# Optimization experiments

Hardware: AMD Instinct MI355X
Metric: run time of the kernel (lower is better)

## Reference

```python
import jax, jax.numpy as jnp
import numpy as np

N_NODES = 50000


def gcn_norm(edge_index, edge_weight, n):
    """PyG GCNConv normalization: add self-loops (weight 1), sym-normalize."""
    src, dst = edge_index[0], edge_index[1]
    loop = jnp.arange(n, dtype=src.dtype)
    src = jnp.concatenate([src, loop])
    dst = jnp.concatenate([dst, loop])
    w = jnp.concatenate([edge_weight, jnp.ones((n,), dtype=edge_weight.dtype)])
    deg = jax.ops.segment_sum(w, dst, num_segments=n)  # in-degree w/ self-loops
    dis = jnp.where(deg > 0, jax.lax.rsqrt(deg), 0.0)  # deg^{-1/2}, inf -> 0
    norm = dis[src] * w * dis[dst]                      # [E+N]
    return src, dst, norm


def gcn_conv(x, src, dst, norm, W, b):
    h = x @ W                                            # [N, F_out]
    msg = norm[:, None] * h[src]                         # gather + scale
    out = jax.ops.segment_sum(msg, dst, num_segments=x.shape[0])  # scatter-add
    return out + b


def setup_inputs() -> dict:
    key = jax.random.key(0)
    ks = jax.random.split(key, 10)
    n, e = N_NODES, 800000
    in_dim, hidden, out_dim = 256, 128, 64
    x = jax.random.normal(ks[0], (n, in_dim), dtype=jnp.float32)
    edge_index = jax.random.randint(ks[1], (2, e), 0, n, dtype=jnp.int32)
    edge_weight = jax.random.uniform(ks[2], (e,), dtype=jnp.float32)
    def glorot(k, fi, fo):
        lim = float(np.sqrt(6.0 / (fi + fo)))
        return jax.random.uniform(k, (fi, fo), minval=-lim, maxval=lim, dtype=jnp.float32)
    return {
        "x": x, "edge_index": edge_index, "edge_weight": edge_weight,
        "W1": glorot(ks[3], in_dim, hidden), "b1": jnp.zeros((hidden,), jnp.float32),
        "W2": glorot(ks[4], hidden, hidden), "b2": jnp.zeros((hidden,), jnp.float32),
        "W3": glorot(ks[5], hidden, out_dim), "b3": jnp.zeros((out_dim,), jnp.float32),
    }


def reference(x, edge_index, edge_weight, W1, b1, W2, b2, W3, b3):
    n = x.shape[0]
    src, dst, norm = gcn_norm(edge_index, edge_weight, n)  # cached=True: shared
    h = jax.nn.relu(gcn_conv(x, src, dst, norm, W1, b1))   # dropout: eval mode no-op
    h = jax.nn.relu(gcn_conv(h, src, dst, norm, W2, b2))
    h = gcn_conv(h, src, dst, norm, W3, b3)
    return h
```

## Files before the change

### kernel.cpp

```cpp
#include <hip/hip_runtime.h>
#include <hip/hip_bf16.h>
#include <stdint.h>

#define NODES 50000
#define EDGES 800000
#define R_REP 8
#define DEG_EPT 4
#define SCAN_TB 256
#define SCAN_NB ((NODES + SCAN_TB - 1) / SCAN_TB)

typedef short bf16x8 __attribute__((ext_vector_type(8)));
typedef float f32x4 __attribute__((ext_vector_type(4)));

__device__ __forceinline__ unsigned short f2bf(float f) {
    union { float f; unsigned u; } v; v.f = f;
    unsigned r = v.u + 0x7fff + ((v.u >> 16) & 1);
    return (unsigned short)(r >> 16);
}
__device__ __forceinline__ float bf2f(unsigned short h) {
    union { float f; unsigned u; } v; v.u = ((unsigned)h) << 16;
    return v.f;
}
__device__ __forceinline__ float bflo(unsigned hv) {
    union { float f; unsigned u; } v; v.u = hv << 16;
    return v.f;
}
__device__ __forceinline__ float bfhi(unsigned hv) {
    union { float f; unsigned u; } v; v.u = hv & 0xffff0000u;
    return v.f;
}


__device__ __forceinline__ void wfrag_one(const float* __restrict__ W, unsigned short* Wf,
                                          int idx, int K, int Nn) {
    int NT = Nn >> 4;
    int lane = idx & 63;
    int f = idx >> 6;
    int nt = f % NT;
    int k0 = (f / NT) << 5;
    int n = (nt << 4) + (lane & 15);
    int kk = k0 + ((lane >> 4) << 3);
    unsigned short o[8];
#pragma unroll
    for (int j = 0; j < 8; j++) o[j] = f2bf(W[(kk + j) * Nn + n]);
    ((uint4*)Wf)[idx] = *(uint4*)o;
}

__global__ void k_setup(unsigned long long* packed,
                        const float* __restrict__ W1, unsigned short* Wf1,
                        const float* __restrict__ W2, unsigned short* Wf2,
                        const float* __restrict__ W3, unsigned short* Wf3) {
    int idx = blockIdx.x * blockDim.x + threadIdx.x;
    if (idx < NODES * R_REP) { packed[idx] = 0ull; return; }
    int k = idx - NODES * R_REP;
    if (k < 4096) wfrag_one(W1, Wf1, k, 256, 128);
    else if (k < 6144) wfrag_one(W2, Wf2, k - 4096, 128, 128);
    else if (k < 7168) wfrag_one(W3, Wf3, k - 6144, 128, 64);
}

__global__ void k_deg(const int* __restrict__ dst, const float* __restrict__ w,
                      unsigned long long* __restrict__ packed, int* __restrict__ rank) {
    int base = blockIdx.x * (256 * DEG_EPT) + threadIdx.x;
    int r = blockIdx.x & (R_REP - 1);
    unsigned long long olds[DEG_EPT];
#pragma unroll
    for (int q = 0; q < DEG_EPT; q++) {
        int e = base + q * 256;
        if (e < EDGES) {
            int d = dst[e];
            unsigned fx = __float2uint_rn(w[e] * 16777216.0f);
            unsigned long long add = (1ull << 40) | (unsigned long long)fx;
            olds[q] = atomicAdd(&packed[(size_t)r * NODES + d], add);
        }
    }
#pragma unroll
    for (int q = 0; q < DEG_EPT; q++) {
        int e = base + q * 256;
        if (e < EDGES) rank[e] = (int)(olds[q] >> 40);
    }
}


__global__ void k_scan1(const unsigned long long* __restrict__ packed,
                        float* __restrict__ dis, int* __restrict__ repoff,
                        int* __restrict__ pre, int* __restrict__ bsum) {
    __shared__ int sm[SCAN_TB];
    int t = threadIdx.x;
    int i = blockIdx.x * SCAN_TB + t;
    int v = 0;
    if (i < NODES) {
        unsigned long long degfx = 0;
        int off = 0;
#pragma unroll
        for (int r = 0; r < R_REP; r++) {
            unsigned long long pk = packed[(size_t)r * NODES + i];
            repoff[(size_t)r * NODES + i] = off;
            off += (int)(pk >> 40);
            degfx += (pk & 0xFFFFFFFFFFull);
        }
        v = off;
        float deg = 1.0f + (float)degfx * (1.0f / 16777216.0f);
        dis[i] = rsqrtf(deg);
    }
    sm[t] = v;
    __syncthreads();
    for (int off = 1; off < SCAN_TB; off <<= 1) {
        int x = (t >= off) ? sm[t - off] : 0;
        __syncthreads();
        sm[t] += x;
        __syncthreads();
    }
    if (i < NODES) pre[i] = sm[t] - v;
    if (t == SCAN_TB - 1) bsum[blockIdx.x] = sm[t];
}

__global__ void k_scan2(const int* __restrict__ bsum, int* __restrict__ boff,
                        int* __restrict__ rowptr) {
    __shared__ int sm[256];
    int t = threadIdx.x;
    int v = (t < SCAN_NB) ? bsum[t] : 0;
    sm[t] = v;
    __syncthreads();
    for (int off = 1; off < 256; off <<= 1) {
        int x = (t >= off) ? sm[t - off] : 0;
        __syncthreads();
        sm[t] += x;
        __syncthreads();
    }
    if (t < SCAN_NB) boff[t] = sm[t] - v;
    if (t == 255) rowptr[NODES] = sm[255];
}

__global__ void k_scatter(const int* __restrict__ src, const int* __restrict__ dst,
                          const float* __restrict__ w, const float* __restrict__ dis,
                          const int* __restrict__ pre, const int* __restrict__ boff,
                          const int* __restrict__ repoff, const int* __restrict__ rank,
                          int2* __restrict__ rec, int* __restrict__ rowptr) {
    int e = blockIdx.x * blockDim.x + threadIdx.x;
    if (e < NODES) rowptr[e] = pre[e] + boff[e >> 8];
    if (e < EDGES) {
        int r = (e >> 10) & (R_REP - 1);
        int s = src[e], d = dst[e];
        float nrm = dis[s] * w[e] * dis[d];
        int pos = pre[d] + boff[d >> 8] + repoff[(size_t)r * NODES + d] + rank[e];
        int2 rc; rc.x = s; rc.y = __float_as_int(nrm);
        rec[pos] = rc;
    }
}

template <int K, int Nn, bool A_F32>
__global__ void k_gemm(const void* __restrict__ A_, const uint4* __restrict__ Wf,
                       unsigned short* __restrict__ Hout) {
    constexpr int NT = Nn / 16;
    int lane = threadIdx.x & 63;
    int wave = threadIdx.x >> 6;
    int tile = blockIdx.x * 4 + wave;
    if (tile * 16 >= NODES) return;
    int row = tile * 16 + (lane & 15);
    int kbase = (lane >> 4) * 8;

    f32x4 acc[NT];
#pragma unroll
    for (int i = 0; i < NT; i++) acc[i] = (f32x4){0.f, 0.f, 0.f, 0.f};

    for (int k0 = 0; k0 < K; k0 += 32) {
        bf16x8 a;
        if (A_F32) {
            const float* A = (const float*)A_;
            const float4* p = (const float4*)&A[(size_t)row * K + k0 + kbase];
            float4 u0 = p[0], u1 = p[1];
            unsigned short t[8];
            t[0] = f2bf(u0.x); t[1] = f2bf(u0.y); t[2] = f2bf(u0.z); t[3] = f2bf(u0.w);
            t[4] = f2bf(u1.x); t[5] = f2bf(u1.y); t[6] = f2bf(u1.z); t[7] = f2bf(u1.w);
            a = *(bf16x8*)t;
        } else {
            const unsigned short* A = (const unsigned short*)A_;
            a = *(const bf16x8*)&A[(size_t)row * K + k0 + kbase];
        }
        int fbase = (k0 >> 5) * NT;
#pragma unroll
        for (int nt = 0; nt < NT; nt++) {
            uint4 braw = Wf[(fbase + nt) * 64 + lane];
            bf16x8 b = *(bf16x8*)&braw;
            acc[nt] = __builtin_amdgcn_mfma_f32_16x16x32_bf16(a, b, acc[nt], 0, 0, 0);
        }
    }
    int r0 = (lane >> 4) * 4;
    int col = lane & 15;
#pragma unroll
    for (int nt = 0; nt < NT; nt++) {
#pragma unroll
        for (int r = 0; r < 4; r++) {
            int m = tile * 16 + r0 + r;
            Hout[(size_t)m * Nn + nt * 16 + col] = f2bf(acc[nt][r]);
        }
    }
}

template <int F, bool RELU, bool OUT_F32>
__global__ void k_agg(const unsigned short* __restrict__ H, const int2* __restrict__ rec,
                      const int* __restrict__ rowptr, const float* __restrict__ dis,
                      const float* __restrict__ bias, void* __restrict__ out_) {
    constexpr int VPT = F / 64;
    int lane = threadIdx.x & 63;
    int node = blockIdx.x * 4 + (threadIdx.x >> 6);
    if (node >= NODES) return;
    node = __builtin_amdgcn_readfirstlane(node);

    const unsigned* H32 = (const unsigned*)H;

    float sn = dis[node]; sn = sn * sn;
    float acc0, acc1 = 0.f;
    if (VPT == 2) {
        unsigned hv = H32[node * 64 + lane];
        acc0 = sn * bflo(hv);
        acc1 = sn * bfhi(hv);
    } else {
        acc0 = sn * bf2f(H[node * 64 + lane]);
    }

    int beg = rowptr[node], end = rowptr[node + 1];
    int last = end - 1;
    for (int j = beg; j < end; j += 8) {
        int ss[8]; float nn[8];
#pragma unroll
        for (int q = 0; q < 8; q++) {
            int idx = j + q;
            idx = (idx < last) ? idx : last;
            int2 rc = rec[idx];
            ss[q] = rc.x;
            nn[q] = (j + q < end) ? __int_as_float(rc.y) : 0.0f;
        }
        if (VPT == 2) {
            unsigned hh[8];
#pragma unroll
            for (int q = 0; q < 8; q++) hh[q] = H32[ss[q] * 64 + lane];
#pragma unroll
            for (int q = 0; q < 8; q++) {
                acc0 += nn[q] * bflo(hh[q]);
                acc1 += nn[q] * bfhi(hh[q]);
            }
        } else {
            unsigned short hh[8];
#pragma unroll
            for (int q = 0; q < 8; q++) hh[q] = H[ss[q] * 64 + lane];
#pragma unroll
            for (int q = 0; q < 8; q++) acc0 += nn[q] * bf2f(hh[q]);
        }
    }

    if (OUT_F32) {
        float* out = (float*)out_;
        if (VPT == 2) {
            float x0 = acc0 + bias[lane * 2];
            float x1 = acc1 + bias[lane * 2 + 1];
            if (RELU) { x0 = fmaxf(x0, 0.f); x1 = fmaxf(x1, 0.f); }
            out[(size_t)node * F + lane * 2] = x0;
            out[(size_t)node * F + lane * 2 + 1] = x1;
        } else {
            float x0 = acc0 + bias[lane];
            if (RELU) x0 = fmaxf(x0, 0.f);
            out[(size_t)node * F + lane] = x0;
        }
    } else {
        unsigned short* out = (unsigned short*)out_;
        if (VPT == 2) {
            float x0 = acc0 + bias[lane * 2];
            float x1 = acc1 + bias[lane * 2 + 1];
            if (RELU) { x0 = fmaxf(x0, 0.f); x1 = fmaxf(x1, 0.f); }
            unsigned packed = (unsigned)f2bf(x0) | ((unsigned)f2bf(x1) << 16);
            *(unsigned*)&out[(size_t)node * F + lane * 2] = packed;
        } else {
            float x0 = acc0 + bias[lane];
            if (RELU) x0 = fmaxf(x0, 0.f);
            out[(size_t)node * F + lane] = f2bf(x0);
        }
    }
}


extern "C" void kernel_launch(void* const* d_in, const int* in_sizes, int n_in,
                              void* d_out, int out_size, void* d_ws, size_t ws_size,
                              hipStream_t stream) {
    const float* x  = (const float*)d_in[0];
    const int*   ei = (const int*)d_in[1];
    const float* w  = (const float*)d_in[2];
    const float* W1 = (const float*)d_in[3];
    const float* b1 = (const float*)d_in[4];
    const float* W2 = (const float*)d_in[5];
    const float* b2 = (const float*)d_in[6];
    const float* W3 = (const float*)d_in[7];
    const float* b3 = (const float*)d_in[8];
    const int* src = ei;
    const int* dst = ei + EDGES;

    char* p = (char*)d_ws;
    auto alloc = [&](size_t n) { char* r = p; p += (n + 511) & ~(size_t)511; return r; };
    unsigned long long* packed = (unsigned long long*)alloc((size_t)NODES * R_REP * 8);
    float*          dis    = (float*)alloc(NODES * 4);
    int*            rowptr = (int*)alloc((NODES + 1) * 4);
    int*            repoff = (int*)alloc((size_t)NODES * R_REP * 4);
    int*            rank   = (int*)alloc(EDGES * 4);
    int*            pre    = (int*)alloc(NODES * 4);
    int*            bsum   = (int*)alloc(SCAN_NB * 4);
    int*            boff   = (int*)alloc(SCAN_NB * 4);
    int2*           rec    = (int2*)alloc(EDGES * 8);
    unsigned short* h      = (unsigned short*)alloc((size_t)NODES * 128 * 2);
    unsigned short* xb     = (unsigned short*)alloc((size_t)NODES * 128 * 2);
    unsigned short* wf1    = (unsigned short*)alloc(256 * 128 * 2);
    unsigned short* wf2    = (unsigned short*)alloc(128 * 128 * 2);
    unsigned short* wf3    = (unsigned short*)alloc(128 * 64 * 2);

    const int TB = 256;
    int nb_setup = (NODES * R_REP + 7168 + TB - 1) / TB;
    int nb_deg   = (EDGES + TB * DEG_EPT - 1) / (TB * DEG_EPT);
    int nb_edges = (EDGES + TB - 1) / TB;

    hipLaunchKernelGGL(k_setup, dim3(nb_setup), dim3(TB), 0, stream, packed, W1, wf1, W2, wf2, W3, wf3);
    hipLaunchKernelGGL(k_deg, dim3(nb_deg), dim3(TB), 0, stream, dst, w, packed, rank);
    hipLaunchKernelGGL(k_scan1, dim3(SCAN_NB), dim3(SCAN_TB), 0, stream, packed, dis, repoff, pre, bsum);
    hipLaunchKernelGGL(k_scan2, dim3(1), dim3(256), 0, stream, bsum, boff, rowptr);
    hipLaunchKernelGGL(k_scatter, dim3(nb_edges), dim3(TB), 0, stream, src, dst, w, dis,
                       pre, boff, repoff, rank, rec, rowptr);

    int nb_gemm = (NODES / 16 + 3) / 4;
    int nb_agg  = (NODES + 3) / 4;

    hipLaunchKernelGGL((k_gemm<256, 128, true>), dim3(nb_gemm), dim3(TB), 0, stream, (const void*)x, (const uint4*)wf1, h);
    hipLaunchKernelGGL((k_agg<128, true, false>), dim3(nb_agg), dim3(TB), 0, stream, h, rec, rowptr, dis, b1, (void*)xb);

    hipLaunchKernelGGL((k_gemm<128, 128, false>), dim3(nb_gemm), dim3(TB), 0, stream, (const void*)xb, (const uint4*)wf2, h);
    hipLaunchKernelGGL((k_agg<128, true, false>), dim3(nb_agg), dim3(TB), 0, stream, h, rec, rowptr, dis, b2, (void*)xb);

    hipLaunchKernelGGL((k_gemm<128, 64, false>), dim3(nb_gemm), dim3(TB), 0, stream, (const void*)xb, (const uint4*)wf3, h);
    hipLaunchKernelGGL((k_agg<64, false, true>), dim3(nb_agg), dim3(TB), 0, stream, h, rec, rowptr, dis, b3, d_out);
}
```

Measured before the change: 292.9 us.

## Fuse degree counting with first GEMM and replace two-pass scan with atomic cursor

```diff
diff --git a/kernel.cpp b/kernel.cpp
--- a/kernel.cpp
+++ b/kernel.cpp
@@ -8,6 +8,8 @@
 #define DEG_EPT 4
 #define SCAN_TB 256
 #define SCAN_NB ((NODES + SCAN_TB - 1) / SCAN_TB)
+#define NVB_DEG ((EDGES + 1023) / 1024)
+#define NVB_GEMM ((NODES / 16 + 3) / 4)
 
 typedef short bf16x8 __attribute__((ext_vector_type(8)));
 typedef float f32x4 __attribute__((ext_vector_type(4)));
@@ -46,11 +48,12 @@
     ((uint4*)Wf)[idx] = *(uint4*)o;
 }
 
-__global__ void k_setup(unsigned long long* packed,
+__global__ void k_setup(unsigned long long* packed, int* cursor,
                         const float* __restrict__ W1, unsigned short* Wf1,
                         const float* __restrict__ W2, unsigned short* Wf2,
                         const float* __restrict__ W3, unsigned short* Wf3) {
     int idx = blockIdx.x * blockDim.x + threadIdx.x;
+    if (idx == 0) *cursor = 0;
     if (idx < NODES * R_REP) { packed[idx] = 0ull; return; }
     int k = idx - NODES * R_REP;
     if (k < 4096) wfrag_one(W1, Wf1, k, 256, 128);
@@ -58,103 +61,14 @@
     else if (k < 7168) wfrag_one(W3, Wf3, k - 6144, 128, 64);
 }
 
-__global__ void k_deg(const int* __restrict__ dst, const float* __restrict__ w,
-                      unsigned long long* __restrict__ packed, int* __restrict__ rank) {
-    int base = blockIdx.x * (256 * DEG_EPT) + threadIdx.x;
-    int r = blockIdx.x & (R_REP - 1);
-    unsigned long long olds[DEG_EPT];
-#pragma unroll
-    for (int q = 0; q < DEG_EPT; q++) {
-        int e = base + q * 256;
-        if (e < EDGES) {
-            int d = dst[e];
-            unsigned fx = __float2uint_rn(w[e] * 16777216.0f);
-            unsigned long long add = (1ull << 40) | (unsigned long long)fx;
-            olds[q] = atomicAdd(&packed[(size_t)r * NODES + d], add);
-        }
-    }
-#pragma unroll
-    for (int q = 0; q < DEG_EPT; q++) {
-        int e = base + q * 256;
-        if (e < EDGES) rank[e] = (int)(olds[q] >> 40);
-    }
-}
-
-
-__global__ void k_scan1(const unsigned long long* __restrict__ packed,
-                        float* __restrict__ dis, int* __restrict__ repoff,
-                        int* __restrict__ pre, int* __restrict__ bsum) {
-    __shared__ int sm[SCAN_TB];
-    int t = threadIdx.x;
-    int i = blockIdx.x * SCAN_TB + t;
-    int v = 0;
-    if (i < NODES) {
-        unsigned long long degfx = 0;
-        int off = 0;
-#pragma unroll
-        for (int r = 0; r < R_REP; r++) {
-            unsigned long long pk = packed[(size_t)r * NODES + i];
-            repoff[(size_t)r * NODES + i] = off;
-            off += (int)(pk >> 40);
-            degfx += (pk & 0xFFFFFFFFFFull);
-        }
-        v = off;
-        float deg = 1.0f + (float)degfx * (1.0f / 16777216.0f);
-        dis[i] = rsqrtf(deg);
-    }
-    sm[t] = v;
-    __syncthreads();
-    for (int off = 1; off < SCAN_TB; off <<= 1) {
-        int x = (t >= off) ? sm[t - off] : 0;
-        __syncthreads();
-        sm[t] += x;
-        __syncthreads();
-    }
-    if (i < NODES) pre[i] = sm[t] - v;
-    if (t == SCAN_TB - 1) bsum[blockIdx.x] = sm[t];
-}
-
-__global__ void k_scan2(const int* __restrict__ bsum, int* __restrict__ boff,
-                        int* __restrict__ rowptr) {
-    __shared__ int sm[256];
-    int t = threadIdx.x;
-    int v = (t < SCAN_NB) ? bsum[t] : 0;
-    sm[t] = v;
-    __syncthreads();
-    for (int off = 1; off < 256; off <<= 1) {
-        int x = (t >= off) ? sm[t - off] : 0;
-        __syncthreads();
-        sm[t] += x;
-        __syncthreads();
-    }
-    if (t < SCAN_NB) boff[t] = sm[t] - v;
-    if (t == 255) rowptr[NODES] = sm[255];
-}
-
-__global__ void k_scatter(const int* __restrict__ src, const int* __restrict__ dst,
-                          const float* __restrict__ w, const float* __restrict__ dis,
-                          const int* __restrict__ pre, const int* __restrict__ boff,
-                          const int* __restrict__ repoff, const int* __restrict__ rank,
-                          int2* __restrict__ rec, int* __restrict__ rowptr) {
-    int e = blockIdx.x * blockDim.x + threadIdx.x;
-    if (e < NODES) rowptr[e] = pre[e] + boff[e >> 8];
-    if (e < EDGES) {
-        int r = (e >> 10) & (R_REP - 1);
-        int s = src[e], d = dst[e];
-        float nrm = dis[s] * w[e] * dis[d];
-        int pos = pre[d] + boff[d >> 8] + repoff[(size_t)r * NODES + d] + rank[e];
-        int2 rc; rc.x = s; rc.y = __float_as_int(nrm);
-        rec[pos] = rc;
-    }
-}
-
 template <int K, int Nn, bool A_F32>
-__global__ void k_gemm(const void* __restrict__ A_, const uint4* __restrict__ Wf,
-                       unsigned short* __restrict__ Hout) {
+__device__ __forceinline__ void gemm_vb(const void* __restrict__ A_,
+                                        const uint4* __restrict__ Wf,
+                                        unsigned short* __restrict__ Hout, int vb) {
     constexpr int NT = Nn / 16;
     int lane = threadIdx.x & 63;
     int wave = threadIdx.x >> 6;
-    int tile = blockIdx.x * 4 + wave;
+    int tile = vb * 4 + wave;
     if (tile * 16 >= NODES) return;
     int row = tile * 16 + (lane & 15);
     int kbase = (lane >> 4) * 8;
@@ -167,8 +81,8 @@
         bf16x8 a;
         if (A_F32) {
             const float* A = (const float*)A_;
-            const float4* p = (const float4*)&A[(size_t)row * K + k0 + kbase];
-            float4 u0 = p[0], u1 = p[1];
+            const float4* pp = (const float4*)&A[(size_t)row * K + k0 + kbase];
+            float4 u0 = pp[0], u1 = pp[1];
             unsigned short t[8];
             t[0] = f2bf(u0.x); t[1] = f2bf(u0.y); t[2] = f2bf(u0.z); t[3] = f2bf(u0.w);
             t[4] = f2bf(u1.x); t[5] = f2bf(u1.y); t[6] = f2bf(u1.z); t[7] = f2bf(u1.w);
@@ -197,9 +111,96 @@
     }
 }
 
+__global__ void k_deg_gemm1(const int* __restrict__ dst, const float* __restrict__ w,
+                            unsigned long long* __restrict__ packed, int* __restrict__ rank,
+                            const float* __restrict__ x, const uint4* __restrict__ Wf1,
+                            unsigned short* __restrict__ h) {
+    int half = blockIdx.x >> 1;
+    if ((blockIdx.x & 1) == 0) {
+        if (half >= NVB_DEG) return;
+        int base = half * 1024 + threadIdx.x;
+        int r = half & (R_REP - 1);
+        unsigned long long olds[DEG_EPT];
+#pragma unroll
+        for (int q = 0; q < DEG_EPT; q++) {
+            int e = base + q * 256;
+            if (e < EDGES) {
+                int d = dst[e];
+                unsigned fx = __float2uint_rn(w[e] * 16777216.0f);
+                unsigned long long add = (1ull << 40) | (unsigned long long)fx;
+                olds[q] = atomicAdd(&packed[(size_t)r * NODES + d], add);
+            }
+        }
+#pragma unroll
+        for (int q = 0; q < DEG_EPT; q++) {
+            int e = base + q * 256;
+            if (e < EDGES) rank[e] = (int)(olds[q] >> 40);
+        }
+    } else {
+        if (half >= NVB_GEMM) return;
+        gemm_vb<256, 128, true>((const void*)x, Wf1, h, half);
+    }
+}
+
+__global__ void k_scan(const unsigned long long* __restrict__ packed,
+                       float* __restrict__ dis, int* __restrict__ repoff,
+                       int2* __restrict__ rsc, int* __restrict__ cursor) {
+    __shared__ int sm[SCAN_TB];
+    __shared__ int s_base;
+    int t = threadIdx.x;
+    int i = blockIdx.x * SCAN_TB + t;
+    int v = 0;
+    if (i < NODES) {
+        unsigned long long degfx = 0;
+        int off = 0;
+#pragma unroll
+        for (int r = 0; r < R_REP; r++) {
+            unsigned long long pk = packed[(size_t)r * NODES + i];
+            repoff[(size_t)r * NODES + i] = off;
+            off += (int)(pk >> 40);
+            degfx += (pk & 0xFFFFFFFFFFull);
+        }
+        v = off;
+        dis[i] = rsqrtf(1.0f + (float)degfx * (1.0f / 16777216.0f));
+    }
+    sm[t] = v;
+    __syncthreads();
+    for (int off = 1; off < SCAN_TB; off <<= 1) {
+        int x2 = (t >= off) ? sm[t - off] : 0;
+        __syncthreads();
+        sm[t] += x2;
+        __syncthreads();
+    }
+    int incl = sm[t];
+    if (t == SCAN_TB - 1) s_base = atomicAdd(cursor, incl);
+    __syncthreads();
+    if (i < NODES) { int2 rs; rs.x = s_base + incl - v; rs.y = v; rsc[i] = rs; }
+}
+
+__global__ void k_scatter(const int* __restrict__ src, const int* __restrict__ dst,
+                          const float* __restrict__ w, const float* __restrict__ dis,
+                          const int2* __restrict__ rsc, const int* __restrict__ repoff,
+                          const int* __restrict__ rank, int2* __restrict__ rec) {
+    int e = blockIdx.x * blockDim.x + threadIdx.x;
+    if (e < EDGES) {
+        int r = (e >> 10) & (R_REP - 1);
+        int s = src[e], d = dst[e];
+        float nrm = dis[s] * w[e] * dis[d];
+        int pos = rsc[d].x + repoff[(size_t)r * NODES + d] + rank[e];
+        int2 rc; rc.x = s; rc.y = __float_as_int(nrm);
+        rec[pos] = rc;
+    }
+}
+
+template <int K, int Nn, bool A_F32>
+__global__ void k_gemm(const void* __restrict__ A_, const uint4* __restrict__ Wf,
+                       unsigned short* __restrict__ Hout) {
+    gemm_vb<K, Nn, A_F32>(A_, Wf, Hout, blockIdx.x);
+}
+
 template <int F, bool RELU, bool OUT_F32>
 __global__ void k_agg(const unsigned short* __restrict__ H, const int2* __restrict__ rec,
-                      const int* __restrict__ rowptr, const float* __restrict__ dis,
+                      const int2* __restrict__ rsc, const float* __restrict__ dis,
                       const float* __restrict__ bias, void* __restrict__ out_) {
     constexpr int VPT = F / 64;
     int lane = threadIdx.x & 63;
@@ -219,7 +220,8 @@
         acc0 = sn * bf2f(H[node * 64 + lane]);
     }
 
-    int beg = rowptr[node], end = rowptr[node + 1];
+    int2 rs = rsc[node];
+    int beg = rs.x, end = rs.x + rs.y;
     int last = end - 1;
     for (int j = beg; j < end; j += 8) {
         int ss[8]; float nn[8];
@@ -268,8 +270,8 @@
             float x0 = acc0 + bias[lane * 2];
             float x1 = acc1 + bias[lane * 2 + 1];
             if (RELU) { x0 = fmaxf(x0, 0.f); x1 = fmaxf(x1, 0.f); }
-            unsigned packed = (unsigned)f2bf(x0) | ((unsigned)f2bf(x1) << 16);
-            *(unsigned*)&out[(size_t)node * F + lane * 2] = packed;
+            unsigned pk = (unsigned)f2bf(x0) | ((unsigned)f2bf(x1) << 16);
+            *(unsigned*)&out[(size_t)node * F + lane * 2] = pk;
         } else {
             float x0 = acc0 + bias[lane];
             if (RELU) x0 = fmaxf(x0, 0.f);
@@ -298,12 +300,10 @@
     auto alloc = [&](size_t n) { char* r = p; p += (n + 511) & ~(size_t)511; return r; };
     unsigned long long* packed = (unsigned long long*)alloc((size_t)NODES * R_REP * 8);
     float*          dis    = (float*)alloc(NODES * 4);
-    int*            rowptr = (int*)alloc((NODES + 1) * 4);
+    int2*           rsc    = (int2*)alloc((size_t)NODES * 8);
     int*            repoff = (int*)alloc((size_t)NODES * R_REP * 4);
     int*            rank   = (int*)alloc(EDGES * 4);
-    int*            pre    = (int*)alloc(NODES * 4);
-    int*            bsum   = (int*)alloc(SCAN_NB * 4);
-    int*            boff   = (int*)alloc(SCAN_NB * 4);
+    int*            cursor = (int*)alloc(4);
     int2*           rec    = (int2*)alloc(EDGES * 8);
     unsigned short* h      = (unsigned short*)alloc((size_t)NODES * 128 * 2);
     unsigned short* xb     = (unsigned short*)alloc((size_t)NODES * 128 * 2);
@@ -313,25 +313,26 @@
 
     const int TB = 256;
     int nb_setup = (NODES * R_REP + 7168 + TB - 1) / TB;
-    int nb_deg   = (EDGES + TB * DEG_EPT - 1) / (TB * DEG_EPT);
+    int nb_fused = 2 * ((NVB_DEG > NVB_GEMM) ? NVB_DEG : NVB_GEMM);
     int nb_edges = (EDGES + TB - 1) / TB;
 
-    hipLaunchKernelGGL(k_setup, dim3(nb_setup), dim3(TB), 0, stream, packed, W1, wf1, W2, wf2, W3, wf3);
-    hipLaunchKernelGGL(k_deg, dim3(nb_deg), dim3(TB), 0, stream, dst, w, packed, rank);
-    hipLaunchKernelGGL(k_scan1, dim3(SCAN_NB), dim3(SCAN_TB), 0, stream, packed, dis, repoff, pre, bsum);
-    hipLaunchKernelGGL(k_scan2, dim3(1), dim3(256), 0, stream, bsum, boff, rowptr);
-    hipLaunchKernelGGL(k_scatter, dim3(nb_edges), dim3(TB), 0, stream, src, dst, w, dis,
-                       pre, boff, repoff, rank, rec, rowptr);
-
-    int nb_gemm = (NODES / 16 + 3) / 4;
+    hipLaunchKernelGGL(k_setup, dim3(nb_setup), dim3(TB), 0, stream,
+                       packed, cursor, W1, wf1, W2, wf2, W3, wf3);
+    hipLaunchKernelGGL(k_deg_gemm1, dim3(nb_fused), dim3(TB), 0, stream,
+                       dst, w, packed, rank, x, (const uint4*)wf1, h);
+    hipLaunchKernelGGL(k_scan, dim3(SCAN_NB), dim3(SCAN_TB), 0, stream,
+                       packed, dis, repoff, rsc, cursor);
+    hipLaunchKernelGGL(k_scatter, dim3(nb_edges), dim3(TB), 0, stream,
+                       src, dst, w, dis, rsc, repoff, rank, rec);
+
+    int nb_gemm = NVB_GEMM;
     int nb_agg  = (NODES + 3) / 4;
 
-    hipLaunchKernelGGL((k_gemm<256, 128, true>), dim3(nb_gemm), dim3(TB), 0, stream, (const void*)x, (const uint4*)wf1, h);
-    hipLaunchKernelGGL((k_agg<128, true, false>), dim3(nb_agg), dim3(TB), 0, stream, h, rec, rowptr, dis, b1, (void*)xb);
+    hipLaunchKernelGGL((k_agg<128, true, false>), dim3(nb_agg), dim3(TB), 0, stream, h, rec, rsc, dis, b1, (void*)xb);
 
     hipLaunchKernelGGL((k_gemm<128, 128, false>), dim3(nb_gemm), dim3(TB), 0, stream, (const void*)xb, (const uint4*)wf2, h);
-    hipLaunchKernelGGL((k_agg<128, true, false>), dim3(nb_agg), dim3(TB), 0, stream, h, rec, rowptr, dis, b2, (void*)xb);
+    hipLaunchKernelGGL((k_agg<128, true, false>), dim3(nb_agg), dim3(TB), 0, stream, h, rec, rsc, dis, b2, (void*)xb);
 
     hipLaunchKernelGGL((k_gemm<128, 64, false>), dim3(nb_gemm), dim3(TB), 0, stream, (const void*)xb, (const uint4*)wf3, h);
-    hipLaunchKernelGGL((k_agg<64, false, true>), dim3(nb_agg), dim3(TB), 0, stream, h, rec, rowptr, dis, b3, d_out);
-}
+    hipLaunchKernelGGL((k_agg<64, false, true>), dim3(nb_agg), dim3(TB), 0, stream, h, rec, rsc, dis, b3, d_out);
+}
```

Result: faster. 276.9 us (-5.5%).
